# Kernel optimization log

Measured on AMD Instinct MI355X. Metric: run time of the kernel, lower is better.

## Reference

```python
import jax, jax.numpy as jnp
import numpy as np

SEQ_LEN = 1000
IN_DIM = 100
POOL = SEQ_LEN // IN_DIM  # 10
HIDDEN = 64
OUT_DIM = 5
N_BASIS = 16
BATCH = 65536


def setup_inputs() -> dict:
    key = jax.random.key(0)
    k1, k2, k3 = jax.random.split(key, 3)
    x = jax.random.normal(k1, (BATCH, SEQ_LEN), dtype=jnp.float32)
    c1_mu = jax.random.normal(k2, (HIDDEN, IN_DIM, N_BASIS), dtype=jnp.float32) * 0.05
    c2_mu = jax.random.normal(k3, (OUT_DIM, HIDDEN, N_BASIS), dtype=jnp.float32) * 0.05
    centers = jnp.linspace(-3.0, 3.0, N_BASIS, dtype=jnp.float32)
    return {"x": x, "c1_mu": c1_mu, "c2_mu": c2_mu, "centers": centers}


def _norm(x):
    # torch .std() uses ddof=1 (unbiased)
    mu = jnp.mean(x, axis=1, keepdims=True)
    sd = jnp.std(x, axis=1, keepdims=True, ddof=1)
    return (x - mu) / (sd + 1e-6)


def _basis(x, centers):
    # x: [b, d] -> [b, d, n_basis]; RBF with fixed variance 0.36
    d = x[..., None] - centers
    return jnp.exp(-0.5 * d * d / 0.36)


def _kan(x, c, centers):
    B = _basis(x, centers)  # [b, i, n]
    return jnp.einsum('bin,oin->bo', B, c)


def reference(x, c1_mu, c2_mu, centers):
    b = x.shape[0]
    # unfold(1, pool, pool).mean(-1): non-overlapping average pooling
    x = x.reshape(b, IN_DIM, POOL).mean(-1)  # [b, 100]
    x = _norm(x)
    h = jnp.tanh(_kan(x, c1_mu, centers))  # [b, 64]
    h = _norm(h)
    out = _kan(h, c2_mu, centers)  # [b, 5]
    return out
```

## Files before the change

### kernel.cpp

```cpp
#include <hip/hip_runtime.h>
#include <hip/hip_bf16.h>


#define SEQ    1000
#define INDIM  100
#define HID    64
#define OUTD   5
#define NB     16
#define ROWS   64
#define NTHR   512

typedef __bf16 v8bf __attribute__((ext_vector_type(8)));
typedef float  v4f  __attribute__((ext_vector_type(4)));

#define RED_OFF 16640
#define R2_OFF  25856
#define B1C_OFF 47360
#define B2C_OFF 58880
#define CEN_OFF 76288
#define SM_BYTES 76352

__global__ __launch_bounds__(256) void cvt_w(
    const float* __restrict__ c1, const float* __restrict__ c2,
    __bf16* __restrict__ c1b, __bf16* __restrict__ c2b)
{
  int t = blockIdx.x * 256 + threadIdx.x;
  if (t < 25600) {
    float4 v = ((const float4*)c1)[t];
    __bf16* d = c1b + t * 4;
    d[0] = (__bf16)v.x; d[1] = (__bf16)v.y; d[2] = (__bf16)v.z; d[3] = (__bf16)v.w;
  }
  if (t < 4096) {
    int o = t >> 8;
    __bf16* d = c2b + t * 4;
    if (o < OUTD) {
      float4 v = ((const float4*)c2)[t];
      d[0] = (__bf16)v.x; d[1] = (__bf16)v.y; d[2] = (__bf16)v.z; d[3] = (__bf16)v.w;
    } else {
      d[0] = (__bf16)0.f; d[1] = (__bf16)0.f; d[2] = (__bf16)0.f; d[3] = (__bf16)0.f;
    }
  }
}

__global__ __launch_bounds__(NTHR, 2) void kan_main(
    const float* __restrict__ x, const __bf16* __restrict__ c1b,
    const __bf16* __restrict__ c2bw, const float* __restrict__ cen,
    float* __restrict__ out)
{
  __shared__ __align__(16) unsigned char sm[SM_BYTES];
  float*  xn  = (float*)sm;
  float*  hb  = (float*)sm;
  float*  red = (float*)(sm + RED_OFF);
  __bf16* c1c = (__bf16*)(sm + R2_OFF);
  __bf16* b1c = (__bf16*)(sm + B1C_OFF);
  __bf16* c2s = (__bf16*)(sm + R2_OFF);
  __bf16* b2c = (__bf16*)(sm + B2C_OFF);
  float*  scen = (float*)(sm + CEN_OFF);

  const int tid  = threadIdx.x;
  const int row0 = blockIdx.x * ROWS;
  if (tid < NB) scen[tid] = cen[tid];

  const float kC = -(0.5f / 0.36f);
  const int w = tid >> 6, lane = tid & 63;
  const int l15 = lane & 15, q = lane >> 4;

  #pragma unroll
  for (int it = 0; it < 13; ++it) {
    int idx = tid + it * NTHR;
    if (idx < 6400) {
      int r = idx / 100, i = idx - r * 100;
      const float2* xp = (const float2*)(x + (size_t)(row0 + r) * SEQ + i * 10);
      float s = 0.f;
      #pragma unroll
      for (int j = 0; j < 5; ++j) { float2 v = xp[j]; s += v.x + v.y; }
      xn[r * 101 + i] = s * 0.1f;
    }
  }
  __syncthreads();

  #pragma unroll
  for (int rr = 0; rr < 8; ++rr) {
    int r = w * 8 + rr;
    float v0 = xn[r * 101 + lane];
    float v1 = (lane < 36) ? xn[r * 101 + 64 + lane] : 0.f;
    float s = v0 + v1, s2 = v0 * v0 + v1 * v1;
    #pragma unroll
    for (int m = 32; m; m >>= 1) { s += __shfl_xor(s, m, 64); s2 += __shfl_xor(s2, m, 64); }
    float mu = s * (1.f / INDIM);
    float var = (s2 - INDIM * mu * mu) * (1.f / (INDIM - 1));
    float rs = 1.f / (sqrtf(fmaxf(var, 0.f)) + 1e-6f);
    xn[r * 101 + lane] = (v0 - mu) * rs;
    if (lane < 36) xn[r * 101 + 64 + lane] = (v1 - mu) * rs;
  }
  __syncthreads();

  const int g = w >> 1;
  const int fh = (w & 1) * 2;
  v4f acc[2];
  acc[0] = (v4f){0.f,0.f,0.f,0.f}; acc[1] = (v4f){0.f,0.f,0.f,0.f};

  for (int c = 0; c < 10; ++c) {
    #pragma unroll
    for (int it = 0; it < 3; ++it) {
      int id2 = tid + it * NTHR;
      if (id2 < 1280) {
        int o = id2 / 20, k16 = id2 - o * 20;
        uint4 v = *(const uint4*)(c1b + (size_t)o * 1600 + c * 160 + k16 * 8);
        *(uint4*)(c1c + o * 168 + k16 * 8) = v;
      }
    }
    #pragma unroll
    for (int it = 0; it < 10; ++it) {
      int idx = tid + it * NTHR;
      int r = idx / 80, pp = idx - r * 80;
      int i = pp >> 3, n = (pp & 7) * 2;
      float xv = xn[r * 101 + c * 10 + i];
      float d0 = xv - scen[n], d1 = xv - scen[n + 1];
      __hip_bfloat162 h2;
      h2.x = __float2bfloat16(__expf(d0 * d0 * kC));
      h2.y = __float2bfloat16(__expf(d1 * d1 * kC));
      *(__hip_bfloat162*)(b1c + r * 168 + pp * 2) = h2;
    }
    __syncthreads();
    const int ar = g * 16 + l15;
    #pragma unroll
    for (int ks = 0; ks < 5; ++ks) {
      v8bf a = *(const v8bf*)&b1c[ar * 168 + ks * 32 + q * 8];
      #pragma unroll
      for (int ff = 0; ff < 2; ++ff) {
        v8bf b = *(const v8bf*)&c1c[((fh + ff) * 16 + l15) * 168 + ks * 32 + q * 8];
        acc[ff] = __builtin_amdgcn_mfma_f32_16x16x32_bf16(a, b, acc[ff], 0, 0, 0);
      }
    }
    __syncthreads();
  }

  #pragma unroll
  for (int ff = 0; ff < 2; ++ff) {
    #pragma unroll
    for (int rg = 0; rg < 4; ++rg) {
      float t = acc[ff][rg];
      float e = __expf(2.f * t);
      hb[(g * 16 + q * 4 + rg) * 65 + (fh + ff) * 16 + l15] = 1.f - 2.f / (e + 1.f);
    }
  }
  __syncthreads();

  #pragma unroll
  for (int rr = 0; rr < 8; ++rr) {
    int r = w * 8 + rr;
    float v = hb[r * 65 + lane];
    float s = v, s2 = v * v;
    #pragma unroll
    for (int m = 32; m; m >>= 1) { s += __shfl_xor(s, m, 64); s2 += __shfl_xor(s2, m, 64); }
    float mu = s * (1.f / HID);
    float var = (s2 - HID * mu * mu) * (1.f / (HID - 1));
    float rs = 1.f / (sqrtf(fmaxf(var, 0.f)) + 1e-6f);
    hb[r * 65 + lane] = (v - mu) * rs;
  }
  #pragma unroll
  for (int it = 0; it < 4; ++it) {
    int idx = tid + it * NTHR;
    int o = idx >> 7, k16 = idx & 127;
    uint4 v = *(const uint4*)(c2bw + o * 1024 + k16 * 8);
    *(uint4*)(c2s + o * 1032 + k16 * 8) = v;
  }
  __syncthreads();

  v4f acc2 = (v4f){0.f,0.f,0.f,0.f};
  for (int c = 0; c < 8; ++c) {
    #pragma unroll
    for (int it = 0; it < 8; ++it) {
      int idx = tid + it * NTHR;
      int r = idx >> 6, pp = idx & 63;
      int i = pp >> 3, n = (pp & 7) * 2;
      float hv = hb[r * 65 + c * 8 + i];
      float d0 = hv - scen[n], d1 = hv - scen[n + 1];
      __hip_bfloat162 h2;
      h2.x = __float2bfloat16(__expf(d0 * d0 * kC));
      h2.y = __float2bfloat16(__expf(d1 * d1 * kC));
      *(__hip_bfloat162*)(b2c + r * 136 + pp * 2) = h2;
    }
    __syncthreads();
    #pragma unroll
    for (int kk = 0; kk < 2; ++kk) {
      int ks = (w & 1) * 2 + kk;
      v8bf a = *(const v8bf*)&b2c[(g * 16 + l15) * 136 + ks * 32 + q * 8];
      v8bf b = *(const v8bf*)&c2s[l15 * 1032 + c * 128 + ks * 32 + q * 8];
      acc2 = __builtin_amdgcn_mfma_f32_16x16x32_bf16(a, b, acc2, 0, 0, 0);
    }
    __syncthreads();
  }

  if (w & 1) {
    #pragma unroll
    for (int rg = 0; rg < 4; ++rg)
      red[(g * 16 + q * 4 + rg) * 17 + l15] = acc2[rg];
  }
  __syncthreads();
  if (!(w & 1) && l15 < OUTD) {
    #pragma unroll
    for (int rg = 0; rg < 4; ++rg) {
      int r = g * 16 + q * 4 + rg;
      out[(size_t)(row0 + r) * OUTD + l15] = acc2[rg] + red[r * 17 + l15];
    }
  }
}

extern "C" void kernel_launch(void* const* d_in, const int* in_sizes, int n_in,
                              void* d_out, int out_size, void* d_ws, size_t ws_size,
                              hipStream_t stream) {
  const float* x   = (const float*)d_in[0];
  const float* c1  = (const float*)d_in[1];
  const float* c2  = (const float*)d_in[2];
  const float* cen = (const float*)d_in[3];
  float* out = (float*)d_out;

  __bf16* c1b = (__bf16*)d_ws;
  __bf16* c2b = (__bf16*)((char*)d_ws + 204800);

  hipLaunchKernelGGL(cvt_w, dim3(100), dim3(256), 0, stream, c1, c2, c1b, c2b);
  hipLaunchKernelGGL(kan_main, dim3(65536 / ROWS), dim3(NTHR), 0, stream,
                     x, c1b, c2b, cen, out);
}
```

Baseline: 421.2 us.

## Use single-wave 16-row blocks computing RBF basis in registers and reading weights from global

Each block now handles 16 rows with one 64-thread wave instead of 64 rows with 8 waves. The RBF basis values are computed directly in registers as MFMA A-operands instead of being staged through LDS, and the bf16 weight tiles are read straight from global/L2 instead of being copied into shared memory. This removes most __syncthreads and LDS traffic and lets many small blocks fill the GPU. In exchange, every block rereads the full weight matrices from cache, and each wave recomputes exp values with a pre-scaled centre trick.

```diff
diff --git a/kernel.cpp b/kernel.cpp
--- a/kernel.cpp
+++ b/kernel.cpp
@@ -7,18 +7,14 @@
 #define HID    64
 #define OUTD   5
 #define NB     16
-#define ROWS   64
-#define NTHR   512
+#define ROWS   16
+#define NTHR   64
 
 typedef __bf16 v8bf __attribute__((ext_vector_type(8)));
 typedef float  v4f  __attribute__((ext_vector_type(4)));
 
-#define RED_OFF 16640
-#define R2_OFF  25856
-#define B1C_OFF 47360
-#define B2C_OFF 58880
-#define CEN_OFF 76288
-#define SM_BYTES 76352
+#define XSTR 101
+#define HSTR 65
 
 __global__ __launch_bounds__(256) void cvt_w(
     const float* __restrict__ c1, const float* __restrict__ c2,
@@ -42,169 +38,132 @@
   }
 }
 
-__global__ __launch_bounds__(NTHR, 2) void kan_main(
+__global__ __launch_bounds__(NTHR, 4) void kan_main(
     const float* __restrict__ x, const __bf16* __restrict__ c1b,
     const __bf16* __restrict__ c2bw, const float* __restrict__ cen,
     float* __restrict__ out)
 {
-  __shared__ __align__(16) unsigned char sm[SM_BYTES];
-  float*  xn  = (float*)sm;
-  float*  hb  = (float*)sm;
-  float*  red = (float*)(sm + RED_OFF);
-  __bf16* c1c = (__bf16*)(sm + R2_OFF);
-  __bf16* b1c = (__bf16*)(sm + B1C_OFF);
-  __bf16* c2s = (__bf16*)(sm + R2_OFF);
-  __bf16* b2c = (__bf16*)(sm + B2C_OFF);
-  float*  scen = (float*)(sm + CEN_OFF);
+  __shared__ __align__(16) float sm[ROWS * XSTR];
+  float* xn = sm;
+  float* hb = sm;
 
   const int tid  = threadIdx.x;
   const int row0 = blockIdx.x * ROWS;
-  if (tid < NB) scen[tid] = cen[tid];
+  const int l15 = tid & 15, q = tid >> 4, iq = q >> 1;
 
-  const float kC = -(0.5f / 0.36f);
-  const int w = tid >> 6, lane = tid & 63;
-  const int l15 = lane & 15, q = lane >> 4;
+  const float Sn = 1.17851130f;
+  float cs[8];
+  {
+    const int n0 = (q & 1) * 8;
+    #pragma unroll
+    for (int j = 0; j < 8; ++j) cs[j] = cen[n0 + j] * Sn;
+  }
 
   #pragma unroll
   for (int it = 0; it < 13; ++it) {
     int idx = tid + it * NTHR;
-    if (idx < 6400) {
-      int r = idx / 100, i = idx - r * 100;
-      const float2* xp = (const float2*)(x + (size_t)(row0 + r) * SEQ + i * 10);
-      float s = 0.f;
-      #pragma unroll
-      for (int j = 0; j < 5; ++j) { float2 v = xp[j]; s += v.x + v.y; }
-      xn[r * 101 + i] = s * 0.1f;
+    if (idx < 800) {
+      int r = idx / 50, p = idx - r * 50;
+      const float4* xp = (const float4*)(x + (size_t)(row0 + r) * SEQ + p * 20);
+      float4 a0 = xp[0], a1 = xp[1], a2 = xp[2], a3 = xp[3], a4 = xp[4];
+      float s0 = a0.x + a0.y + a0.z + a0.w + a1.x + a1.y + a1.z + a1.w + a2.x + a2.y;
+      float s1 = a2.z + a2.w + a3.x + a3.y + a3.z + a3.w + a4.x + a4.y + a4.z + a4.w;
+      xn[r * XSTR + 2 * p]     = s0 * 0.1f;
+      xn[r * XSTR + 2 * p + 1] = s1 * 0.1f;
     }
   }
   __syncthreads();
 
   #pragma unroll
-  for (int rr = 0; rr < 8; ++rr) {
-    int r = w * 8 + rr;
-    float v0 = xn[r * 101 + lane];
-    float v1 = (lane < 36) ? xn[r * 101 + 64 + lane] : 0.f;
+  for (int rr = 0; rr < 16; ++rr) {
+    float v0 = xn[rr * XSTR + tid];
+    float v1 = (tid < 36) ? xn[rr * XSTR + 64 + tid] : 0.f;
     float s = v0 + v1, s2 = v0 * v0 + v1 * v1;
     #pragma unroll
     for (int m = 32; m; m >>= 1) { s += __shfl_xor(s, m, 64); s2 += __shfl_xor(s2, m, 64); }
     float mu = s * (1.f / INDIM);
     float var = (s2 - INDIM * mu * mu) * (1.f / (INDIM - 1));
     float rs = 1.f / (sqrtf(fmaxf(var, 0.f)) + 1e-6f);
-    xn[r * 101 + lane] = (v0 - mu) * rs;
-    if (lane < 36) xn[r * 101 + 64 + lane] = (v1 - mu) * rs;
+    xn[rr * XSTR + tid] = (v0 - mu) * rs;
+    if (tid < 36) xn[rr * XSTR + 64 + tid] = (v1 - mu) * rs;
   }
   __syncthreads();
 
-  const int g = w >> 1;
-  const int fh = (w & 1) * 2;
-  v4f acc[2];
-  acc[0] = (v4f){0.f,0.f,0.f,0.f}; acc[1] = (v4f){0.f,0.f,0.f,0.f};
+  const float* xrow = xn + l15 * XSTR;
+  const __bf16* bp0 = c1b + (size_t)(l15)      * 1600 + q * 8;
+  const __bf16* bp1 = c1b + (size_t)(16 + l15) * 1600 + q * 8;
+  const __bf16* bp2 = c1b + (size_t)(32 + l15) * 1600 + q * 8;
+  const __bf16* bp3 = c1b + (size_t)(48 + l15) * 1600 + q * 8;
+  v4f acc0 = {0.f, 0.f, 0.f, 0.f}, acc1 = acc0, acc2 = acc0, acc3 = acc0;
 
+  #pragma unroll 2
   for (int c = 0; c < 10; ++c) {
     #pragma unroll
-    for (int it = 0; it < 3; ++it) {
-      int id2 = tid + it * NTHR;
-      if (id2 < 1280) {
-        int o = id2 / 20, k16 = id2 - o * 20;
-        uint4 v = *(const uint4*)(c1b + (size_t)o * 1600 + c * 160 + k16 * 8);
-        *(uint4*)(c1c + o * 168 + k16 * 8) = v;
+    for (int ks = 0; ks < 5; ++ks) {
+      int ko = c * 160 + ks * 32;
+      float xv = xrow[c * 10 + 2 * ks + iq] * Sn;
+      v8bf a;
+      #pragma unroll
+      for (int j = 0; j < 8; ++j) {
+        float d = xv - cs[j];
+        a[j] = (__bf16)__expf(-(d * d));
       }
-    }
-    #pragma unroll
-    for (int it = 0; it < 10; ++it) {
-      int idx = tid + it * NTHR;
-      int r = idx / 80, pp = idx - r * 80;
-      int i = pp >> 3, n = (pp & 7) * 2;
-      float xv = xn[r * 101 + c * 10 + i];
-      float d0 = xv - scen[n], d1 = xv - scen[n + 1];
-      __hip_bfloat162 h2;
-      h2.x = __float2bfloat16(__expf(d0 * d0 * kC));
-      h2.y = __float2bfloat16(__expf(d1 * d1 * kC));
-      *(__hip_bfloat162*)(b1c + r * 168 + pp * 2) = h2;
-    }
-    __syncthreads();
-    const int ar = g * 16 + l15;
-    #pragma unroll
-    for (int ks = 0; ks < 5; ++ks) {
-      v8bf a = *(const v8bf*)&b1c[ar * 168 + ks * 32 + q * 8];
-      #pragma unroll
-      for (int ff = 0; ff < 2; ++ff) {
-        v8bf b = *(const v8bf*)&c1c[((fh + ff) * 16 + l15) * 168 + ks * 32 + q * 8];
-        acc[ff] = __builtin_amdgcn_mfma_f32_16x16x32_bf16(a, b, acc[ff], 0, 0, 0);
-      }
-    }
-    __syncthreads();
-  }
-
-  #pragma unroll
-  for (int ff = 0; ff < 2; ++ff) {
-    #pragma unroll
-    for (int rg = 0; rg < 4; ++rg) {
-      float t = acc[ff][rg];
-      float e = __expf(2.f * t);
-      hb[(g * 16 + q * 4 + rg) * 65 + (fh + ff) * 16 + l15] = 1.f - 2.f / (e + 1.f);
+      v8bf b0 = *(const v8bf*)(bp0 + ko);
+      v8bf b1 = *(const v8bf*)(bp1 + ko);
+      v8bf b2 = *(const v8bf*)(bp2 + ko);
+      v8bf b3 = *(const v8bf*)(bp3 + ko);
+      acc0 = __builtin_amdgcn_mfma_f32_16x16x32_bf16(a, b0, acc0, 0, 0, 0);
+      acc1 = __builtin_amdgcn_mfma_f32_16x16x32_bf16(a, b1, acc1, 0, 0, 0);
+      acc2 = __builtin_amdgcn_mfma_f32_16x16x32_bf16(a, b2, acc2, 0, 0, 0);
+      acc3 = __builtin_amdgcn_mfma_f32_16x16x32_bf16(a, b3, acc3, 0, 0, 0);
     }
   }
   __syncthreads();
 
+  auto tanh_store = [&](v4f a, int cb) {
+    #pragma unroll
+    for (int rg = 0; rg < 4; ++rg) {
+      float t = a[rg];
+      float e = __expf(t + t);
+      hb[(q * 4 + rg) * HSTR + cb * 16 + l15] = 1.f - 2.f / (e + 1.f);
+    }
+  };
+  tanh_store(acc0, 0); tanh_store(acc1, 1); tanh_store(acc2, 2); tanh_store(acc3, 3);
+  __syncthreads();
+
   #pragma unroll
-  for (int rr = 0; rr < 8; ++rr) {
-    int r = w * 8 + rr;
-    float v = hb[r * 65 + lane];
+  for (int rr = 0; rr < 16; ++rr) {
+    float v = hb[rr * HSTR + tid];
     float s = v, s2 = v * v;
     #pragma unroll
     for (int m = 32; m; m >>= 1) { s += __shfl_xor(s, m, 64); s2 += __shfl_xor(s2, m, 64); }
     float mu = s * (1.f / HID);
     float var = (s2 - HID * mu * mu) * (1.f / (HID - 1));
     float rs = 1.f / (sqrtf(fmaxf(var, 0.f)) + 1e-6f);
-    hb[r * 65 + lane] = (v - mu) * rs;
-  }
-  #pragma unroll
-  for (int it = 0; it < 4; ++it) {
-    int idx = tid + it * NTHR;
-    int o = idx >> 7, k16 = idx & 127;
-    uint4 v = *(const uint4*)(c2bw + o * 1024 + k16 * 8);
-    *(uint4*)(c2s + o * 1032 + k16 * 8) = v;
+    hb[rr * HSTR + tid] = (v - mu) * rs;
   }
   __syncthreads();
 
-  v4f acc2 = (v4f){0.f,0.f,0.f,0.f};
-  for (int c = 0; c < 8; ++c) {
+  const float* hrow = hb + l15 * HSTR;
+  const __bf16* bp4 = c2bw + (size_t)l15 * 1024 + q * 8;
+  v4f o4 = {0.f, 0.f, 0.f, 0.f};
+  #pragma unroll 8
+  for (int t8 = 0; t8 < 32; ++t8) {
+    float hv = hrow[2 * t8 + iq] * Sn;
+    v8bf a;
     #pragma unroll
-    for (int it = 0; it < 8; ++it) {
-      int idx = tid + it * NTHR;
-      int r = idx >> 6, pp = idx & 63;
-      int i = pp >> 3, n = (pp & 7) * 2;
-      float hv = hb[r * 65 + c * 8 + i];
-      float d0 = hv - scen[n], d1 = hv - scen[n + 1];
-      __hip_bfloat162 h2;
-      h2.x = __float2bfloat16(__expf(d0 * d0 * kC));
-      h2.y = __float2bfloat16(__expf(d1 * d1 * kC));
-      *(__hip_bfloat162*)(b2c + r * 136 + pp * 2) = h2;
+    for (int j = 0; j < 8; ++j) {
+      float d = hv - cs[j];
+      a[j] = (__bf16)__expf(-(d * d));
     }
-    __syncthreads();
-    #pragma unroll
-    for (int kk = 0; kk < 2; ++kk) {
-      int ks = (w & 1) * 2 + kk;
-      v8bf a = *(const v8bf*)&b2c[(g * 16 + l15) * 136 + ks * 32 + q * 8];
-      v8bf b = *(const v8bf*)&c2s[l15 * 1032 + c * 128 + ks * 32 + q * 8];
-      acc2 = __builtin_amdgcn_mfma_f32_16x16x32_bf16(a, b, acc2, 0, 0, 0);
-    }
-    __syncthreads();
+    v8bf vb = *(const v8bf*)(bp4 + t8 * 32);
+    o4 = __builtin_amdgcn_mfma_f32_16x16x32_bf16(a, vb, o4, 0, 0, 0);
   }
 
-  if (w & 1) {
+  if (l15 < OUTD) {
     #pragma unroll
     for (int rg = 0; rg < 4; ++rg)
-      red[(g * 16 + q * 4 + rg) * 17 + l15] = acc2[rg];
-  }
-  __syncthreads();
-  if (!(w & 1) && l15 < OUTD) {
-    #pragma unroll
-    for (int rg = 0; rg < 4; ++rg) {
-      int r = g * 16 + q * 4 + rg;
-      out[(size_t)(row0 + r) * OUTD + l15] = acc2[rg] + red[r * 17 + l15];
-    }
+      out[(size_t)(row0 + q * 4 + rg) * OUTD + l15] = o4[rg];
   }
 }
 
```

After: 461.1 us. 1.09x slower.
